# Kernel optimization log

Measured on AMD Instinct MI355X. Metric: run time of the kernel, lower is better.

## Reference

```python
import jax, jax.numpy as jnp
import numpy as np

B, T, C, H = 4, 2048, 1024, 16
HD = C // H  # head dim = 64


def setup_inputs() -> dict:
    key = jax.random.key(0)
    k1, k2, k3 = jax.random.split(key, 3)
    scale_in = 1.0 / np.sqrt(C)
    return {
        "x": jax.random.normal(k1, (B, T, C), dtype=jnp.float32),
        "W_attn": jax.random.normal(k2, (C, 3 * C), dtype=jnp.float32) * scale_in,
        "b_attn": jnp.zeros((3 * C,), dtype=jnp.float32),
        "W_proj": jax.random.normal(k3, (C, C), dtype=jnp.float32) * scale_in,
        "b_proj": jnp.zeros((C,), dtype=jnp.float32),
    }


def reference(x, W_attn, b_attn, W_proj, b_proj):
    b, t, c = x.shape
    qkv = x @ W_attn + b_attn                      # [B,T,3C]
    q, k, v = jnp.split(qkv, 3, axis=-1)
    # [B,T,C] -> [B,H,T,HD]
    def heads(z):
        return z.reshape(b, t, H, HD).transpose(0, 2, 1, 3)
    q, k, v = heads(q), heads(k), heads(v)
    att = jnp.einsum("bhqd,bhkd->bhqk", q, k) / jnp.sqrt(jnp.float32(HD))
    causal = jnp.tril(jnp.ones((t, t), dtype=bool))
    att = jnp.where(causal, att, -jnp.inf)
    att = jax.nn.softmax(att, axis=-1)             # dropout p=0 -> identity
    y = jnp.einsum("bhqk,bhkd->bhqd", att, v)      # [B,H,T,HD]
    y = y.transpose(0, 2, 1, 3).reshape(b, t, c)   # [B,T,C]
    return y @ W_proj + b_proj
```

## Files before the change

### kernel.cpp

```cpp
#include <hip/hip_runtime.h>
#include <hip/hip_bf16.h>

typedef unsigned int u32;
typedef unsigned short u16;
typedef __bf16 bf16x8 __attribute__((ext_vector_type(8)));
typedef float f32x4 __attribute__((ext_vector_type(4)));
typedef _Float16 f16;
typedef _Float16 f16x2 __attribute__((ext_vector_type(2)));
typedef _Float16 f16x4 __attribute__((ext_vector_type(4)));

#define B_ 4
#define T_ 2048
#define C_ 1024
#define H_ 16
#define HD_ 64
#define M_ (B_*T_)
#define N3C (3*C_)
#define N2C (2*C_)

__device__ __forceinline__ u16 f2bf(float f) {
  u32 u = __builtin_bit_cast(u32, f);
  u = (u + 0x7fffu + ((u >> 16) & 1u)) >> 16;
  return (u16)u;
}

#define GLD16(gp, lp) __builtin_amdgcn_global_load_lds( \
    (const __attribute__((address_space(1))) u32*)(gp), \
    (__attribute__((address_space(3))) u32*)(lp), 16, 0, 0)

#if __has_builtin(__builtin_amdgcn_exp2f)
#define EXP2F(x) __builtin_amdgcn_exp2f(x)
#else
#define EXP2F(x) exp2f(x)
#endif

__global__ __launch_bounds__(256) void prep(
    const float* __restrict__ x, const float* __restrict__ Wa,
    const float* __restrict__ Wp,
    u16* __restrict__ xb, u16* __restrict__ W1t, u16* __restrict__ W2t) {
  __shared__ float t[32][33];
  const int blk = blockIdx.x, tid = threadIdx.x;
  if (blk < 8192) {
    int i = blk * 256 + tid;
    float4 v = ((const float4*)x)[i];
    ushort4 o;
    o.x = f2bf(v.x); o.y = f2bf(v.y); o.z = f2bf(v.z); o.w = f2bf(v.w);
    ((ushort4*)xb)[i] = o;
    return;
  }
  const float* W; u16* Wt; int Ndim, id;
  if (blk < 8192 + 3072) { W = Wa; Wt = W1t; Ndim = N3C; id = blk - 8192; }
  else                   { W = Wp; Wt = W2t; Ndim = C_;  id = blk - 11264; }
  const int nt = Ndim / 32;
  const int n0 = (id % nt) * 32, k0 = (id / nt) * 32;
  const int tx = tid & 31, ty = tid >> 5;
  #pragma unroll
  for (int i = ty; i < 32; i += 8)
    t[i][tx] = W[(long)(k0 + i) * Ndim + n0 + tx];
  __syncthreads();
  #pragma unroll
  for (int i = ty; i < 32; i += 8)
    Wt[(long)(n0 + i) * C_ + k0 + tx] = f2bf(t[tx][i]);
}

template<int MODE>
__global__ __launch_bounds__(256) void gemm_bt(
    const u16* __restrict__ A, const u16* __restrict__ Bt,
    const float* __restrict__ bias, void* __restrict__ Cout,
    f16* __restrict__ vt, int N, int K) {
  __shared__ u16 As[128 * 64];
  __shared__ u16 Bs[128 * 64];
  const int tid = threadIdx.x;
  const int wave = tid >> 6, lane = tid & 63;
  const int wm = wave >> 1, wn = wave & 1;
  const int l15 = lane & 15, quad = lane >> 4;
  const int rA = lane >> 3, cxor = (lane & 7) ^ rA;
  const long rowA0 = (long)blockIdx.x * 128;
  const long colB0 = (long)blockIdx.y * 128;

  f32x4 acc[4][4] = {};

  const u16* Ag = A + (rowA0 + wave * 32 + rA) * K + cxor * 8;
  const u16* Bg = Bt + (colB0 + wave * 32 + rA) * K + cxor * 8;
  u16* Asw = &As[(wave * 32) * 64];
  u16* Bsw = &Bs[(wave * 32) * 64];

  const int fbase = l15 * 64 + ((quad ^ (l15 & 3)) << 3) + (((l15 >> 2) & 1) << 5);
  const int aA0 = wm * 4096 + fbase, aA1 = aA0 ^ 32;
  const int bA0 = wn * 4096 + fbase, bA1 = bA0 ^ 32;

  for (int k0 = 0; k0 < K; k0 += 64) {
    #pragma unroll
    for (int j = 0; j < 4; ++j) {
      GLD16(Ag + (long)j * 8 * K + k0, Asw + j * 8 * 64);
      GLD16(Bg + (long)j * 8 * K + k0, Bsw + j * 8 * 64);
    }
    __syncthreads();
    #pragma unroll
    for (int kk = 0; kk < 2; ++kk) {
      const int ai = kk ? aA1 : aA0;
      const int bi = kk ? bA1 : bA0;
      bf16x8 af[4], bfr[4];
      #pragma unroll
      for (int mt = 0; mt < 4; ++mt)
        af[mt] = *(const bf16x8*)&As[ai + mt * 1024];
      #pragma unroll
      for (int nt = 0; nt < 4; ++nt)
        bfr[nt] = *(const bf16x8*)&Bs[bi + nt * 1024];
      #pragma unroll
      for (int mt = 0; mt < 4; ++mt)
        #pragma unroll
        for (int nt = 0; nt < 4; ++nt)
          acc[mt][nt] = __builtin_amdgcn_mfma_f32_16x16x32_bf16(
              af[mt], bfr[nt], acc[mt][nt], 0, 0, 0);
    }
    __syncthreads();
  }

  float bl[4];
  #pragma unroll
  for (int nt = 0; nt < 4; ++nt)
    bl[nt] = bias[colB0 + wn * 64 + nt * 16 + l15];

  const bool vmode = (MODE == 1) && (colB0 >= N2C);
  #pragma unroll
  for (int mt = 0; mt < 4; ++mt) {
    long row = rowA0 + wm * 64 + mt * 16 + quad * 4;
    #pragma unroll
    for (int nt = 0; nt < 4; ++nt) {
      long col = colB0 + wn * 64 + nt * 16 + l15;
      float v0 = acc[mt][nt][0] + bl[nt];
      float v1 = acc[mt][nt][1] + bl[nt];
      float v2 = acc[mt][nt][2] + bl[nt];
      float v3 = acc[mt][nt][3] + bl[nt];
      if (MODE == 0) {
        float* Cf = (float*)Cout;
        Cf[(row + 0) * N + col] = v0;
        Cf[(row + 1) * N + col] = v1;
        Cf[(row + 2) * N + col] = v2;
        Cf[(row + 3) * N + col] = v3;
      } else if (!vmode) {
        u16* qkp = (u16*)Cout;
        qkp[(row + 0) * N2C + col] = f2bf(v0);
        qkp[(row + 1) * N2C + col] = f2bf(v1);
        qkp[(row + 2) * N2C + col] = f2bf(v2);
        qkp[(row + 3) * N2C + col] = f2bf(v3);
      } else {
        int cv = (int)(col - N2C);
        int hh = cv >> 6, dd = cv & 63;
        int bb = (int)(row >> 11);
        long t = row & 2047;
        f16x2 lo = __builtin_bit_cast(f16x2, __builtin_amdgcn_cvt_pkrtz(v0, v1));
        f16x2 hi = __builtin_bit_cast(f16x2, __builtin_amdgcn_cvt_pkrtz(v2, v3));
        f16x4 w; w[0] = lo[0]; w[1] = lo[1]; w[2] = hi[0]; w[3] = hi[1];
        *(f16x4*)&vt[(((long)bb * H_ + hh) * HD_ + dd) * T_ + t] = w;
      }
    }
  }
}

__global__ __launch_bounds__(256, 5) void flash_attn(
    const u16* __restrict__ qk, const f16* __restrict__ vt,
    u16* __restrict__ yb) {
  __shared__ u16 KsF[2 * 64 * 64];
  __shared__ f16 VsF[2 * 64 * 64];
  const int l = blockIdx.x;
  const int bh = (l & 7) | ((l >> 7) << 3);
  const int bx = (l >> 3) & 15;
  const int b = bh >> 4, h = bh & 15;
  const int tid = threadIdx.x, wave = tid >> 6, lane = tid & 63;
  const int l15 = lane & 15, quad = lane >> 4;
  const int rA = lane >> 3, cxor = (lane & 7) ^ rA;

  const u16* Qb = qk + (long)b * T_ * N2C + h * HD_;
  const f16* Vbase = vt + (long)bh * HD_ * T_;
  const u16* Kb0 = Qb + C_ + (long)(wave * 16 + rA) * N2C + cxor * 8;
  const f16* Vb0 = Vbase + (long)(wave * 16 + rA) * T_ + cxor * 8;

  u16* ksw0 = &KsF[(wave * 16) * 64];
  u16* ksw1 = &KsF[4096 + (wave * 16) * 64];
  f16* vsw0 = &VsF[(wave * 16) * 64];
  f16* vsw1 = &VsF[4096 + (wave * 16) * 64];

  const int kA0 = l15 * 64 + ((quad ^ (l15 & 3)) << 3) + (((l15 >> 2) & 1) << 5);
  const int kA1 = kA0 ^ 32;
  const int vA0 = l15 * 64 + (((quad >> 1) ^ (l15 & 7)) << 3) + ((quad & 1) << 2);

  const float cs = 0.125f * 1.44269504088896340736f;

#define FA_TILE(KT, BUF) do {                                                  \
    __syncthreads();                         \
    if ((KT) + 1 < nKT) {                                                      \
      u16* kd = (BUF) ? ksw0 : ksw1;                                           \
      f16* vd = (BUF) ? vsw0 : vsw1;                                           \
      GLD16(kp, kd);                                                           \
      GLD16(kp + 8 * N2C, kd + 8 * 64);                                        \
      GLD16(vp, vd);                                                           \
      GLD16(vp + 8 * T_, vd + 8 * 64);                                         \
      kp += 64 * N2C;                                                          \
      vp += 64;                                                                \
    }                                                                          \
    f32x4 St[4] = {};                                                          \
    _Pragma("unroll")                                                          \
    for (int kk = 0; kk < 2; ++kk) {                                           \
      bf16x8 qf = kk ? bq1 : bq0;                                              \
      const int ki = ((kk ? kA1 : kA0)) + (BUF) * 4096;                        \
      _Pragma("unroll")                                                        \
      for (int mt = 0; mt < 4; ++mt) {                                         \
        bf16x8 kf = *(const bf16x8*)&KsF[ki + mt * 1024];                      \
        St[mt] = __builtin_amdgcn_mfma_f32_16x16x32_bf16(kf, qf, St[mt],       \
                                                         0, 0, 0);             \
      }                                                                        \
    }                                                                          \
    if ((KT) == qt) {                                                          \
      _Pragma("unroll")                                                        \
      for (int mt = 0; mt < 4; ++mt)                                           \
        _Pragma("unroll")                                                      \
        for (int r = 0; r < 4; ++r)                                            \
          if (mt * 16 + quad * 4 + r > wave * 16 + l15)                        \
            St[mt][r] = -__builtin_inff();                                     \
    }                                                                          \
    float ps = 0.f;                                                            \
    f16x4 pf[4];                                                               \
    _Pragma("unroll")                                                          \
    for (int mt = 0; mt < 4; ++mt) {                                           \
      float p0 = EXP2F(__builtin_fmaf(St[mt][0], cs, nref));                   \
      float p1 = EXP2F(__builtin_fmaf(St[mt][1], cs, nref));                   \
      float p2 = EXP2F(__builtin_fmaf(St[mt][2], cs, nref));                   \
      float p3 = EXP2F(__builtin_fmaf(St[mt][3], cs, nref));                   \
      ps += (p0 + p1) + (p2 + p3);                                             \
      f16x2 lo = __builtin_bit_cast(f16x2, __builtin_amdgcn_cvt_pkrtz(p0, p1));\
      f16x2 hi = __builtin_bit_cast(f16x2, __builtin_amdgcn_cvt_pkrtz(p2, p3));\
      pf[mt][0] = lo[0]; pf[mt][1] = lo[1];                                    \
      pf[mt][2] = hi[0]; pf[mt][3] = hi[1];                                    \
    }                                                                          \
    li += ps;                                                                  \
    _Pragma("unroll")                                                          \
    for (int kc = 0; kc < 4; ++kc) {                                           \
      const int vi = (vA0 ^ (kc << 4)) + (BUF) * 4096;                         \
      _Pragma("unroll")                                                        \
      for (int dt = 0; dt < 4; ++dt) {                                         \
        f16x4 vf = *(const f16x4*)&VsF[vi + dt * 1024];                        \
        o[dt] = __builtin_amdgcn_mfma_f32_16x16x16f16(vf, pf[kc], o[dt],       \
                                                      0, 0, 0);               \
      }                                                                        \
    }                                                                          \
  } while (0)

  #pragma unroll 1
  for (int pass = 0; pass < 2; ++pass) {
    const int qt = pass ? bx : 31 - bx;
    const int nKT = qt + 1;
    const int qrow = qt * 64 + wave * 16 + l15;
    const bf16x8 bq0 = *(const bf16x8*)&Qb[(long)qrow * N2C + quad * 8];
    const bf16x8 bq1 = *(const bf16x8*)&Qb[(long)qrow * N2C + 32 + quad * 8];

    float qq = 0.f;
    #pragma unroll
    for (int j = 0; j < 8; ++j) {
      float a = (float)bq0[j], bv = (float)bq1[j];
      qq = __builtin_fmaf(a, a, qq);
      qq = __builtin_fmaf(bv, bv, qq);
    }
    qq += __shfl_xor(qq, 16);
    qq += __shfl_xor(qq, 32);
    const float nref = -qq * cs;

    const u16* kp = Kb0;
    const f16* vp = Vb0;

    __syncthreads();
    GLD16(kp, ksw0);
    GLD16(kp + 8 * N2C, ksw0 + 8 * 64);
    GLD16(vp, vsw0);
    GLD16(vp + 8 * T_, vsw0 + 8 * 64);
    kp += 64 * N2C;
    vp += 64;

    float li = 0.f;
    f32x4 o[4] = {};

    int kt = 0;
    #pragma unroll 1
    for (; kt + 1 < nKT; kt += 2) {
      FA_TILE(kt, 0);
      FA_TILE(kt + 1, 1);
    }
    if (nKT & 1) FA_TILE(nKT - 1, 0);

    li += __shfl_xor(li, 16);
    li += __shfl_xor(li, 32);
    float inv = 1.f / li;
    #pragma unroll
    for (int dt = 0; dt < 4; ++dt) {
      ushort4 w;
      w.x = f2bf(o[dt][0] * inv);
      w.y = f2bf(o[dt][1] * inv);
      w.z = f2bf(o[dt][2] * inv);
      w.w = f2bf(o[dt][3] * inv);
      *(ushort4*)&yb[((long)b * T_ + qrow) * C_ + h * HD_ + dt * 16 + quad * 4] = w;
    }
  }
#undef FA_TILE
}

extern "C" void kernel_launch(void* const* d_in, const int* in_sizes, int n_in,
                              void* d_out, int out_size, void* d_ws, size_t ws_size,
                              hipStream_t stream) {
  const float* x      = (const float*)d_in[0];
  const float* W_attn = (const float*)d_in[1];
  const float* b_attn = (const float*)d_in[2];
  const float* W_proj = (const float*)d_in[3];
  const float* b_proj = (const float*)d_in[4];
  float* out = (float*)d_out;

  char* ws = (char*)d_ws;
  u16* xb   = (u16*)(ws);
  u16* W1t  = (u16*)(ws + 16777216);
  u16* W2t  = (u16*)(ws + 23068672);
  u16* qkb  = (u16*)(ws + 25165824);
  f16* vtb  = (f16*)(ws + 58720256);
  u16* yb   = (u16*)(ws + 75497472);

  prep<<<dim3(12288), dim3(256), 0, stream>>>(x, W_attn, W_proj, xb, W1t, W2t);
  gemm_bt<1><<<dim3(M_ / 128, N3C / 128), dim3(256), 0, stream>>>(
      xb, W1t, b_attn, qkb, vtb, N3C, C_);
  flash_attn<<<dim3(1024), dim3(256), 0, stream>>>(qkb, vtb, yb);
  gemm_bt<0><<<dim3(M_ / 128, C_ / 128), dim3(256), 0, stream>>>(
      yb, W2t, b_proj, out, nullptr, C_, C_);
}
```

Baseline: 246.5 us.

## Split attention into one q-tile per block and use narrower proj GEMM tiles

The flash attention kernel previously paired a long and a short query tile in one block for load balance. It now launches one block per (batch-head, query tile), 2048 blocks ordered longest-first, so the hardware scheduler does the balancing. The projection GEMM gets its own kernel with 128x64 tiles, doubling the block count (512 to 1024) to fill more CUs on a small GEMM. This trades per-block reuse and extra prologue Q loads for better occupancy and tail behavior.

```diff
diff --git a/kernel.cpp b/kernel.cpp
--- a/kernel.cpp
+++ b/kernel.cpp
@@ -63,11 +63,10 @@
     Wt[(long)(n0 + i) * C_ + k0 + tx] = f2bf(t[tx][i]);
 }
 
-template<int MODE>
-__global__ __launch_bounds__(256) void gemm_bt(
+__global__ __launch_bounds__(256) void gemm_qkv(
     const u16* __restrict__ A, const u16* __restrict__ Bt,
-    const float* __restrict__ bias, void* __restrict__ Cout,
-    f16* __restrict__ vt, int N, int K) {
+    const float* __restrict__ bias, u16* __restrict__ qkout,
+    f16* __restrict__ vt) {
   __shared__ u16 As[128 * 64];
   __shared__ u16 Bs[128 * 64];
   const int tid = threadIdx.x;
@@ -77,6 +76,7 @@
   const int rA = lane >> 3, cxor = (lane & 7) ^ rA;
   const long rowA0 = (long)blockIdx.x * 128;
   const long colB0 = (long)blockIdx.y * 128;
+  const int K = C_;
 
   f32x4 acc[4][4] = {};
 
@@ -122,7 +122,7 @@
   for (int nt = 0; nt < 4; ++nt)
     bl[nt] = bias[colB0 + wn * 64 + nt * 16 + l15];
 
-  const bool vmode = (MODE == 1) && (colB0 >= N2C);
+  const bool vmode = (colB0 >= N2C);
   #pragma unroll
   for (int mt = 0; mt < 4; ++mt) {
     long row = rowA0 + wm * 64 + mt * 16 + quad * 4;
@@ -133,18 +133,11 @@
       float v1 = acc[mt][nt][1] + bl[nt];
       float v2 = acc[mt][nt][2] + bl[nt];
       float v3 = acc[mt][nt][3] + bl[nt];
-      if (MODE == 0) {
-        float* Cf = (float*)Cout;
-        Cf[(row + 0) * N + col] = v0;
-        Cf[(row + 1) * N + col] = v1;
-        Cf[(row + 2) * N + col] = v2;
-        Cf[(row + 3) * N + col] = v3;
-      } else if (!vmode) {
-        u16* qkp = (u16*)Cout;
-        qkp[(row + 0) * N2C + col] = f2bf(v0);
-        qkp[(row + 1) * N2C + col] = f2bf(v1);
-        qkp[(row + 2) * N2C + col] = f2bf(v2);
-        qkp[(row + 3) * N2C + col] = f2bf(v3);
+      if (!vmode) {
+        qkout[(row + 0) * N2C + col] = f2bf(v0);
+        qkout[(row + 1) * N2C + col] = f2bf(v1);
+        qkout[(row + 2) * N2C + col] = f2bf(v2);
+        qkout[(row + 3) * N2C + col] = f2bf(v3);
       } else {
         int cv = (int)(col - N2C);
         int hh = cv >> 6, dd = cv & 63;
@@ -159,14 +152,84 @@
   }
 }
 
+__global__ __launch_bounds__(256) void gemm_proj(
+    const u16* __restrict__ A, const u16* __restrict__ Bt,
+    const float* __restrict__ bias, float* __restrict__ Cout) {
+  __shared__ u16 As[128 * 64];
+  __shared__ u16 Bs[64 * 64];
+  const int tid = threadIdx.x;
+  const int wave = tid >> 6, lane = tid & 63;
+  const int l15 = lane & 15, quad = lane >> 4;
+  const int rA = lane >> 3, cxor = (lane & 7) ^ rA;
+  const long rowA0 = (long)blockIdx.x * 128;
+  const long colB0 = (long)blockIdx.y * 64;
+  const int K = C_;
+
+  f32x4 acc[2][4] = {};
+
+  const u16* Ag = A + (rowA0 + wave * 32 + rA) * K + cxor * 8;
+  const u16* Bg = Bt + (colB0 + wave * 16 + rA) * K + cxor * 8;
+  u16* Asw = &As[(wave * 32) * 64];
+  u16* Bsw = &Bs[(wave * 16) * 64];
+
+  const int fbase = l15 * 64 + ((quad ^ (l15 & 3)) << 3) + (((l15 >> 2) & 1) << 5);
+  const int aA0 = wave * 2048 + fbase, aA1 = aA0 ^ 32;
+  const int bA0 = fbase, bA1 = bA0 ^ 32;
+
+  for (int k0 = 0; k0 < K; k0 += 64) {
+    #pragma unroll
+    for (int j = 0; j < 4; ++j)
+      GLD16(Ag + (long)j * 8 * K + k0, Asw + j * 8 * 64);
+    #pragma unroll
+    for (int j = 0; j < 2; ++j)
+      GLD16(Bg + (long)j * 8 * K + k0, Bsw + j * 8 * 64);
+    __syncthreads();
+    #pragma unroll
+    for (int kk = 0; kk < 2; ++kk) {
+      const int ai = kk ? aA1 : aA0;
+      const int bi = kk ? bA1 : bA0;
+      bf16x8 af[2], bfr[4];
+      #pragma unroll
+      for (int mt = 0; mt < 2; ++mt)
+        af[mt] = *(const bf16x8*)&As[ai + mt * 1024];
+      #pragma unroll
+      for (int nt = 0; nt < 4; ++nt)
+        bfr[nt] = *(const bf16x8*)&Bs[bi + nt * 1024];
+      #pragma unroll
+      for (int mt = 0; mt < 2; ++mt)
+        #pragma unroll
+        for (int nt = 0; nt < 4; ++nt)
+          acc[mt][nt] = __builtin_amdgcn_mfma_f32_16x16x32_bf16(
+              af[mt], bfr[nt], acc[mt][nt], 0, 0, 0);
+    }
+    __syncthreads();
+  }
+
+  float bl[4];
+  #pragma unroll
+  for (int nt = 0; nt < 4; ++nt)
+    bl[nt] = bias[colB0 + nt * 16 + l15];
+  #pragma unroll
+  for (int mt = 0; mt < 2; ++mt) {
+    long row = rowA0 + wave * 32 + mt * 16 + quad * 4;
+    #pragma unroll
+    for (int nt = 0; nt < 4; ++nt) {
+      long col = colB0 + nt * 16 + l15;
+      #pragma unroll
+      for (int r = 0; r < 4; ++r)
+        Cout[(row + r) * C_ + col] = acc[mt][nt][r] + bl[nt];
+    }
+  }
+}
+
 __global__ __launch_bounds__(256, 5) void flash_attn(
     const u16* __restrict__ qk, const f16* __restrict__ vt,
     u16* __restrict__ yb) {
   __shared__ u16 KsF[2 * 64 * 64];
   __shared__ f16 VsF[2 * 64 * 64];
   const int l = blockIdx.x;
-  const int bh = (l & 7) | ((l >> 7) << 3);
-  const int bx = (l >> 3) & 15;
+  const int bh = l & 63;
+  const int qt = 31 - (l >> 6);
   const int b = bh >> 4, h = bh & 15;
   const int tid = threadIdx.x, wave = tid >> 6, lane = tid & 63;
   const int l15 = lane & 15, quad = lane >> 4;
@@ -247,59 +310,54 @@
     }                                                                          \
   } while (0)
 
+  const int nKT = qt + 1;
+  const int qrow = qt * 64 + wave * 16 + l15;
+  const bf16x8 bq0 = *(const bf16x8*)&Qb[(long)qrow * N2C + quad * 8];
+  const bf16x8 bq1 = *(const bf16x8*)&Qb[(long)qrow * N2C + 32 + quad * 8];
+
+  float qq = 0.f;
+  #pragma unroll
+  for (int j = 0; j < 8; ++j) {
+    float a = (float)bq0[j], bv = (float)bq1[j];
+    qq = __builtin_fmaf(a, a, qq);
+    qq = __builtin_fmaf(bv, bv, qq);
+  }
+  qq += __shfl_xor(qq, 16);
+  qq += __shfl_xor(qq, 32);
+  const float nref = -qq * cs;
+
+  const u16* kp = Kb0;
+  const f16* vp = Vb0;
+
+  GLD16(kp, ksw0);
+  GLD16(kp + 8 * N2C, ksw0 + 8 * 64);
+  GLD16(vp, vsw0);
+  GLD16(vp + 8 * T_, vsw0 + 8 * 64);
+  kp += 64 * N2C;
+  vp += 64;
+
+  float li = 0.f;
+  f32x4 o[4] = {};
+
+  int kt = 0;
   #pragma unroll 1
-  for (int pass = 0; pass < 2; ++pass) {
-    const int qt = pass ? bx : 31 - bx;
-    const int nKT = qt + 1;
-    const int qrow = qt * 64 + wave * 16 + l15;
-    const bf16x8 bq0 = *(const bf16x8*)&Qb[(long)qrow * N2C + quad * 8];
-    const bf16x8 bq1 = *(const bf16x8*)&Qb[(long)qrow * N2C + 32 + quad * 8];
-
-    float qq = 0.f;
-    #pragma unroll
-    for (int j = 0; j < 8; ++j) {
-      float a = (float)bq0[j], bv = (float)bq1[j];
-      qq = __builtin_fmaf(a, a, qq);
-      qq = __builtin_fmaf(bv, bv, qq);
-    }
-    qq += __shfl_xor(qq, 16);
-    qq += __shfl_xor(qq, 32);
-    const float nref = -qq * cs;
-
-    const u16* kp = Kb0;
-    const f16* vp = Vb0;
-
-    __syncthreads();
-    GLD16(kp, ksw0);
-    GLD16(kp + 8 * N2C, ksw0 + 8 * 64);
-    GLD16(vp, vsw0);
-    GLD16(vp + 8 * T_, vsw0 + 8 * 64);
-    kp += 64 * N2C;
-    vp += 64;
-
-    float li = 0.f;
-    f32x4 o[4] = {};
-
-    int kt = 0;
-    #pragma unroll 1
-    for (; kt + 1 < nKT; kt += 2) {
-      FA_TILE(kt, 0);
-      FA_TILE(kt + 1, 1);
-    }
-    if (nKT & 1) FA_TILE(nKT - 1, 0);
-
-    li += __shfl_xor(li, 16);
-    li += __shfl_xor(li, 32);
-    float inv = 1.f / li;
-    #pragma unroll
-    for (int dt = 0; dt < 4; ++dt) {
-      ushort4 w;
-      w.x = f2bf(o[dt][0] * inv);
-      w.y = f2bf(o[dt][1] * inv);
-      w.z = f2bf(o[dt][2] * inv);
-      w.w = f2bf(o[dt][3] * inv);
-      *(ushort4*)&yb[((long)b * T_ + qrow) * C_ + h * HD_ + dt * 16 + quad * 4] = w;
-    }
+  for (; kt + 1 < nKT; kt += 2) {
+    FA_TILE(kt, 0);
+    FA_TILE(kt + 1, 1);
+  }
+  if (nKT & 1) FA_TILE(nKT - 1, 0);
+
+  li += __shfl_xor(li, 16);
+  li += __shfl_xor(li, 32);
+  float inv = 1.f / li;
+  #pragma unroll
+  for (int dt = 0; dt < 4; ++dt) {
+    ushort4 w;
+    w.x = f2bf(o[dt][0] * inv);
+    w.y = f2bf(o[dt][1] * inv);
+    w.z = f2bf(o[dt][2] * inv);
+    w.w = f2bf(o[dt][3] * inv);
+    *(ushort4*)&yb[((long)b * T_ + qrow) * C_ + h * HD_ + dt * 16 + quad * 4] = w;
   }
 #undef FA_TILE
 }
@@ -323,9 +381,9 @@
   u16* yb   = (u16*)(ws + 75497472);
 
   prep<<<dim3(12288), dim3(256), 0, stream>>>(x, W_attn, W_proj, xb, W1t, W2t);
-  gemm_bt<1><<<dim3(M_ / 128, N3C / 128), dim3(256), 0, stream>>>(
-      xb, W1t, b_attn, qkb, vtb, N3C, C_);
-  flash_attn<<<dim3(1024), dim3(256), 0, stream>>>(qkb, vtb, yb);
-  gemm_bt<0><<<dim3(M_ / 128, C_ / 128), dim3(256), 0, stream>>>(
-      yb, W2t, b_proj, out, nullptr, C_, C_);
-}
+  gemm_qkv<<<dim3(M_ / 128, N3C / 128), dim3(256), 0, stream>>>(
+      xb, W1t, b_attn, qkb, vtb);
+  flash_attn<<<dim3(2048), dim3(256), 0, stream>>>(qkb, vtb, yb);
+  gemm_proj<<<dim3(M_ / 128, C_ / 64), dim3(256), 0, stream>>>(
+      yb, W2t, b_proj, out);
+}
```

Measured after the change: 238.4 us. 1.03x faster.
